# Performance work log

Hardware: AMD Instinct MI355X
Metric: run time of the kernel (lower is better)

Reference implementation:

```python
import jax, jax.numpy as jnp
import numpy as np

KH, KW = 3, 3
KK = KH * KW
PAD = 1
STRIDE = 1


def setup_inputs() -> dict:
    key = jax.random.key(0)
    k1, k2, k3 = jax.random.split(key, 3)
    x = jax.random.normal(k1, (4, 64, 224, 224), jnp.float32)
    weight = jax.random.normal(k2, (64, 64, KH, KW), jnp.float32) * 0.05
    bias = jax.random.normal(k3, (64,), jnp.float32)
    return {"x": x, "weight": weight, "bias": bias}


def reference(x, weight, bias):
    B, C, H, W = x.shape
    # --- conv output (the wrapper delegates this to the wrapped conv) ---
    y = jax.lax.conv_general_dilated(
        x, weight,
        window_strides=(STRIDE, STRIDE),
        padding=((PAD, PAD), (PAD, PAD)),
        dimension_numbers=("NCHW", "OIHW", "NCHW"),
    ) + bias[None, :, None, None]

    # --- zero-count histogram (groups=1; torch code's [:, :, :, 0, 0] indexing
    # selects group 0 / out-channel 0, so only weight[0] matters) ---
    # patches: (B, C*KK, Ho, Wo), channel-major ordering (channel, then kh, kw)
    patches = jax.lax.conv_general_dilated_patches(
        x, (KH, KW), (STRIDE, STRIDE), ((PAD, PAD), (PAD, PAD)))
    Ho, Wo = patches.shape[2], patches.shape[3]
    patches = patches.reshape(B, C, KK, Ho, Wo)
    prod = patches * weight[0].reshape(1, C, KK, 1, 1)  # patch * weight, oc=0
    # num_of_zeros = kk - count_nonzero over the kernel window
    zeros = KK - jnp.count_nonzero(prod, axis=2)  # (B, C, Ho, Wo), int
    # accumulate one_hot(zeros).sum over (batch, h, w) per input channel
    zf = zeros.transpose(1, 0, 2, 3).reshape(C, -1)  # (C, B*Ho*Wo)
    hist = jnp.zeros((C, KK + 1), jnp.float32).at[
        jnp.arange(C)[:, None], zf].add(1.0)
    return y, hist
```

## Files before the change

kernel.cpp:

```cpp
#include <hip/hip_runtime.h>

#define HW 224
#define HW2 50176
#define NCH 64
#define NPIX (4 * HW2)
#define CONV_OUT_ELEMS (4 * NCH * HW2)
#define ZCAP 8192

typedef short bf16x8 __attribute__((ext_vector_type(8)));
typedef float f32x4 __attribute__((ext_vector_type(4)));

__device__ __forceinline__ unsigned short f2bf(float f) {
    unsigned u = __float_as_uint(f);
    u += 0x7FFFu + ((u >> 16) & 1u);
    return (unsigned short)(u >> 16);
}


__global__ __launch_bounds__(256) void prep_weights_v2(
    const float* __restrict__ w, unsigned short* __restrict__ wbufA,
    int* __restrict__ zcnt) {
    const int o = blockIdx.x * 256 + threadIdx.x;
    if (o == 0) *zcnt = 0;
    if (o >= 18 * 2048) return;
    const int j    = o & 7;
    const int lane = (o >> 3) & 63;
    const int n    = lane & 15;
    const int q    = lane >> 4;
    const int mg   = (o >> 9) & 3;
    const int k    = o >> 11;
    const int tap  = k >> 1;
    const int half = k & 1;
    const int ci   = half * 32 + q * 8 + j;
    const int co   = mg * 16 + n;
    wbufA[o] = f2bf(w[(co * 64 + ci) * 9 + tap]);
}

__global__ __launch_bounds__(256, 3) void conv_fused(
    const float* __restrict__ xf,
    const unsigned short* __restrict__ wbufA,
    const float* __restrict__ bias, float* __restrict__ y,
    int* __restrict__ zcnt, unsigned int* __restrict__ zlist)
{
    __shared__ alignas(16) unsigned short xs[340 * 64];

    const int tid  = threadIdx.x;
    const int wv   = tid >> 6;
    const int lane = tid & 63;
    const int n    = lane & 15;
    const int q    = lane >> 4;
    const int c0   = blockIdx.x * 32;
    const int r0   = blockIdx.y * 8;
    const int b    = blockIdx.z;

    float fv[11][8];
#pragma unroll
    for (int it = 0; it < 11; ++it) {
        const int i   = tid + it * 256;
        const int ii  = i < 2720 ? i : 2719;
        const int oct = ii / 340;
        const int pos = ii - oct * 340;
        const int rr  = pos / 34;
        const int cc  = pos - rr * 34;
        const int gy  = r0 + rr - 1;
        const int gx  = c0 + cc - 1;
        const int cgy = min(max(gy, 0), HW - 1);
        const int cgx = min(max(gx, 0), HW - 1);
        const float* p =
            xf + ((size_t)(b * NCH + oct * 8) * HW + cgy) * HW + cgx;
#pragma unroll
        for (int j = 0; j < 8; ++j) fv[it][j] = p[(size_t)j * HW2];
    }
    __builtin_amdgcn_sched_barrier(0);

#pragma unroll
    for (int it = 0; it < 11; ++it) {
        const int i = tid + it * 256;
        if (i < 2720) {
            const int oct = i / 340;
            const int pos = i - oct * 340;
            const int rr  = pos / 34;
            const int cc  = pos - rr * 34;
            const int gy  = r0 + rr - 1;
            const int gx  = c0 + cc - 1;
            const bool inb =
                (unsigned)gy < (unsigned)HW && (unsigned)gx < (unsigned)HW;
            bf16x8 v;
            bool anyz = false;
#pragma unroll
            for (int j = 0; j < 8; ++j) {
                const float f = inb ? fv[it][j] : 0.0f;
                v[j] = (short)f2bf(f);
                anyz |= (f == 0.0f);
            }
            const int phys = pos * 8 + (oct ^ (pos & 7));
            *reinterpret_cast<bf16x8*>(xs + phys * 8) = v;
            if (__builtin_expect(
                    anyz && rr >= 1 && rr <= 8 && cc >= 1 && cc <= 32, 0)) {
#pragma unroll
                for (int j = 0; j < 8; ++j) {
                    if (fv[it][j] == 0.0f) {
                        const int idx = atomicAdd(zcnt, 1);
                        if (idx < ZCAP) {
                            const int ci = oct * 8 + j;
                            zlist[idx] = ((unsigned)b << 22)
                                       | ((unsigned)ci << 16)
                                       | ((unsigned)gy << 8) | (unsigned)gx;
                        }
                    }
                }
            }
        }
    }
    __syncthreads();

    f32x4 acc[4][4];
#pragma unroll
    for (int mg = 0; mg < 4; ++mg)
#pragma unroll
        for (int g = 0; g < 4; ++g) acc[mg][g] = (f32x4){0.f, 0.f, 0.f, 0.f};

#pragma unroll
    for (int tap = 0; tap < 9; ++tap) {
        const int dh = tap / 3, dw = tap % 3;
#pragma unroll
        for (int half = 0; half < 2; ++half) {
            const int k = tap * 2 + half;
            bf16x8 a[4];
#pragma unroll
            for (int mg = 0; mg < 4; ++mg)
                a[mg] = *reinterpret_cast<const bf16x8*>(
                    wbufA + (k * 4 + mg) * 512 + lane * 8);
#pragma unroll
            for (int g = 0; g < 4; ++g) {
                const int pos = (2 * wv + (g >> 1) + dh) * 34
                              + (g & 1) * 16 + dw + n;
                const int phys = pos * 8 + ((half * 4 + q) ^ (pos & 7));
                const bf16x8 bf =
                    *reinterpret_cast<const bf16x8*>(xs + phys * 8);
#pragma unroll
                for (int mg = 0; mg < 4; ++mg)
                    acc[mg][g] = __builtin_amdgcn_mfma_f32_16x16x32_bf16(
                        a[mg], bf, acc[mg][g], 0, 0, 0);
            }
        }
    }

#pragma unroll
    for (int g = 0; g < 4; ++g) {
        const int row = r0 + 2 * wv + (g >> 1);
        const int col = c0 + (g & 1) * 16 + n;
#pragma unroll
        for (int mg = 0; mg < 4; ++mg) {
#pragma unroll
            for (int rg = 0; rg < 4; ++rg) {
                const int co = mg * 16 + q * 4 + rg;
                y[((size_t)(b * NCH + co) * HW + row) * HW + col] =
                    acc[mg][g][rg] + bias[co];
            }
        }
    }
}

__global__ __launch_bounds__(256) void hist_final(
    const float* __restrict__ x, const float* __restrict__ w,
    const int* __restrict__ zcnt, const unsigned int* __restrict__ zlist,
    float* __restrict__ hist)
{
    __shared__ int lh[640];
    const int tid = threadIdx.x;
    for (int i = tid; i < 640; i += 256) lh[i] = 0;
    __syncthreads();

    if (tid < 64) {
        const int c = tid;
        float wk[9];
#pragma unroll
        for (int k = 0; k < 9; ++k) wk[k] = w[c * 9 + k];
        int bins[10];
#pragma unroll
        for (int k = 0; k < 10; ++k) bins[k] = 0;
#pragma unroll
        for (int rcat = 0; rcat < 3; ++rcat) {
#pragma unroll
            for (int scat = 0; scat < 3; ++scat) {
                int z = 0;
#pragma unroll
                for (int k = 0; k < 9; ++k) {
                    const int kh = k / 3, kw = k % 3;
                    const bool oob =
                        (rcat == 0 && kh == 0) || (rcat == 2 && kh == 2) ||
                        (scat == 0 && kw == 0) || (scat == 2 && kw == 2);
                    z += (oob || wk[k] == 0.0f) ? 1 : 0;
                }
                const int cnt =
                    4 * (rcat == 1 ? 222 : 1) * (scat == 1 ? 222 : 1);
                bins[z] += cnt;
            }
        }
#pragma unroll
        for (int k = 0; k < 10; ++k) lh[c * 10 + k] = bins[k];
    }
    __syncthreads();

    const int L = min(*zcnt, ZCAP);
    for (int p = tid; p < L * 9; p += 256) {
        const int e = p / 9, t = p - e * 9;
        const unsigned ent = zlist[e];
        const int b  = (int)(ent >> 22);
        const int c  = (int)(ent >> 16) & 63;
        const int zy = (int)(ent >> 8) & 255;
        const int zx = (int)ent & 255;
        const int kh = t / 3, kw = t % 3;
        const int r = zy - kh + 1, s = zx - kw + 1;
        if ((unsigned)r >= (unsigned)HW || (unsigned)s >= (unsigned)HW)
            continue;
        bool first = true;
        for (int e2 = 0; e2 < e && first; ++e2) {
            const unsigned ent2 = zlist[e2];
            if ((ent2 >> 16) == (ent >> 16)) {
                const int y2 = (int)(ent2 >> 8) & 255;
                const int x2 = (int)ent2 & 255;
                if ((unsigned)(y2 - r + 1) < 3u && (unsigned)(x2 - s + 1) < 3u)
                    first = false;
            }
        }
        if (!first) continue;

        const float* plane = x + (size_t)(b * NCH + c) * HW2;
        int zb = 0, zt = 0;
#pragma unroll
        for (int k = 0; k < 9; ++k) {
            const int kh2 = k / 3, kw2 = k % 3;
            const int yy = r + kh2 - 1, xx = s + kw2 - 1;
            const bool oob = (unsigned)yy >= (unsigned)HW ||
                             (unsigned)xx >= (unsigned)HW;
            const bool w0 = (w[c * 9 + k] == 0.0f);
            const bool x0 = !oob && (plane[yy * HW + xx] == 0.0f);
            zb += (oob || w0) ? 1 : 0;
            zt += (oob || w0 || x0) ? 1 : 0;
        }
        if (zb != zt) {
            atomicAdd(&lh[c * 10 + zb], -1);
            atomicAdd(&lh[c * 10 + zt], 1);
        }
    }
    __syncthreads();
    for (int i = tid; i < 640; i += 256) hist[i] = (float)lh[i];
}

__global__ void prep_weights_fb(const float* __restrict__ w,
                                unsigned short* __restrict__ wbuf) {
    const int o = blockIdx.x * 256 + threadIdx.x;
    if (o >= 2 * 9 * 4 * 16 * 32) return;
    const int ci = o & 31;
    const int t1 = o >> 5;
    const int co = t1 & 15;
    const int t2 = t1 >> 4;
    const int mg = t2 & 3;
    const int t3 = t2 >> 2;
    const int tap = t3 % 9;
    const int chunk = t3 / 9;
    wbuf[o] = f2bf(w[((mg * 16 + co) * 64 + (chunk * 32 + ci)) * 9 + tap]);
}

__global__ __launch_bounds__(256, 2) void conv_mfma_fb(
    const float* __restrict__ x, const unsigned short* __restrict__ wbuf,
    const float* __restrict__ bias, float* __restrict__ y)
{
    __shared__ alignas(16) unsigned short xs[340 * 32];
    const int tid  = threadIdx.x;
    const int wv   = tid >> 6;
    const int lane = tid & 63;
    const int n    = lane & 15;
    const int q    = lane >> 4;
    const int c0   = blockIdx.x * 32;
    const int r0   = blockIdx.y * 8;
    const int b    = blockIdx.z;

    f32x4 acc[4][4];
#pragma unroll
    for (int mg = 0; mg < 4; ++mg)
#pragma unroll
        for (int g = 0; g < 4; ++g) acc[mg][g] = (f32x4){0.f, 0.f, 0.f, 0.f};

    for (int chunk = 0; chunk < 2; ++chunk) {
        if (chunk) __syncthreads();
        const int ci0 = chunk * 32;
        for (int i = tid; i < 1360; i += 256) {
            const int ci8 = i / 340;
            const int pos = i - ci8 * 340;
            const int r   = pos / 34;
            const int c   = pos - r * 34;
            const int gy  = r0 + r - 1;
            const int gx  = c0 + c - 1;
            bf16x8 v;
            if ((unsigned)gy < (unsigned)HW && (unsigned)gx < (unsigned)HW) {
                const float* src =
                    x + ((size_t)(b * NCH + ci0 + ci8 * 8) * HW + gy) * HW + gx;
#pragma unroll
                for (int j = 0; j < 8; ++j) v[j] = (short)f2bf(src[(size_t)j * HW2]);
            } else {
#pragma unroll
                for (int j = 0; j < 8; ++j) v[j] = 0;
            }
            *reinterpret_cast<bf16x8*>(&xs[pos * 32 + ci8 * 8]) = v;
        }
        __syncthreads();

#pragma unroll
        for (int tap = 0; tap < 9; ++tap) {
            const int dh = tap / 3, dw = tap % 3;
            bf16x8 a[4];
#pragma unroll
            for (int mg = 0; mg < 4; ++mg) {
                const unsigned short* ap =
                    wbuf + ((chunk * 9 + tap) * 4 + mg) * 512 + n * 32 + q * 8;
                a[mg] = *reinterpret_cast<const bf16x8*>(ap);
            }
#pragma unroll
            for (int g = 0; g < 4; ++g) {
                const int rl = 2 * wv + (g >> 1) + dh;
                const int cl = (g & 1) * 16 + dw + n;
                const bf16x8 bf =
                    *reinterpret_cast<const bf16x8*>(&xs[(rl * 34 + cl) * 32 + q * 8]);
#pragma unroll
                for (int mg = 0; mg < 4; ++mg)
                    acc[mg][g] = __builtin_amdgcn_mfma_f32_16x16x32_bf16(
                        a[mg], bf, acc[mg][g], 0, 0, 0);
            }
        }
    }

#pragma unroll
    for (int g = 0; g < 4; ++g) {
        const int row = r0 + 2 * wv + (g >> 1);
        const int col = c0 + (g & 1) * 16 + n;
#pragma unroll
        for (int mg = 0; mg < 4; ++mg) {
#pragma unroll
            for (int rg = 0; rg < 4; ++rg) {
                const int co = mg * 16 + q * 4 + rg;
                y[((size_t)(b * NCH + co) * HW + row) * HW + col] =
                    acc[mg][g][rg] + bias[co];
            }
        }
    }
}

__global__ __launch_bounds__(256) void hist_v2(
    const float* __restrict__ x, const float* __restrict__ w,
    float* __restrict__ hist)
{
    __shared__ int lh[10];
    const int tid = threadIdx.x;
    const int col = tid;
    const int rg  = blockIdx.x;
    const int c   = blockIdx.y;
    const int b   = blockIdx.z;
    if (tid < 10) lh[tid] = 0;
    __syncthreads();

    int h[10];
#pragma unroll
    for (int k = 0; k < 10; ++k) h[k] = 0;

    if (col < HW) {
        const float* plane = x + (size_t)(b * NCH + c) * HW2;
        float wk[9];
#pragma unroll
        for (int k = 0; k < 9; ++k) wk[k] = w[c * 9 + k];

        const bool vl = col > 0, vr = col < HW - 1;
        const int r0 = rg * 28;
        float u0, u1, u2, m0, m1, m2;
        if (r0 > 0) {
            const float* p = plane + (size_t)(r0 - 1) * HW + col;
            u0 = vl ? p[-1] : 0.f; u1 = p[0]; u2 = vr ? p[1] : 0.f;
        } else { u0 = u1 = u2 = 0.f; }
        {
            const float* p = plane + (size_t)r0 * HW + col;
            m0 = vl ? p[-1] : 0.f; m1 = p[0]; m2 = vr ? p[1] : 0.f;
        }

        for (int r = r0; r < r0 + 28; ++r) {
            float d0, d1, d2;
            if (r + 1 < HW) {
                const float* p = plane + (size_t)(r + 1) * HW + col;
                d0 = vl ? p[-1] : 0.f; d1 = p[0]; d2 = vr ? p[1] : 0.f;
            } else { d0 = d1 = d2 = 0.f; }

            int cnt = 0;
            cnt += (u0 * wk[0] != 0.f); cnt += (u1 * wk[1] != 0.f); cnt += (u2 * wk[2] != 0.f);
            cnt += (m0 * wk[3] != 0.f); cnt += (m1 * wk[4] != 0.f); cnt += (m2 * wk[5] != 0.f);
            cnt += (d0 * wk[6] != 0.f); cnt += (d1 * wk[7] != 0.f); cnt += (d2 * wk[8] != 0.f);
            const int z = 9 - cnt;
#pragma unroll
            for (int k = 0; k < 10; ++k) h[k] += (z == k);
            u0 = m0; u1 = m1; u2 = m2; m0 = d0; m1 = d1; m2 = d2;
        }
    }

#pragma unroll
    for (int k = 0; k < 10; ++k) {
        int v = h[k];
        v += __shfl_xor(v, 32); v += __shfl_xor(v, 16); v += __shfl_xor(v, 8);
        v += __shfl_xor(v, 4);  v += __shfl_xor(v, 2);  v += __shfl_xor(v, 1);
        if ((tid & 63) == 0 && v != 0) atomicAdd(&lh[k], v);
    }
    __syncthreads();
    if (tid < 10 && lh[tid] > 0)
        atomicAdd(&hist[c * 10 + tid], (float)lh[tid]);
}

extern "C" void kernel_launch(void* const* d_in, const int* in_sizes, int n_in,
                              void* d_out, int out_size, void* d_ws, size_t ws_size,
                              hipStream_t stream) {
    const float* x    = (const float*)d_in[0];
    const float* w    = (const float*)d_in[1];
    const float* bias = (const float*)d_in[2];
    float* y    = (float*)d_out;
    float* hist = (float*)d_out + CONV_OUT_ELEMS;

    const size_t ZC_OFF = 73728;
    const size_t ZL_OFF = ZC_OFF + 64;
    const size_t NEED   = ZL_OFF + (size_t)ZCAP * 4;

    if (ws_size >= NEED) {
        unsigned short* wbufA = (unsigned short*)d_ws;
        int* zcnt             = (int*)((char*)d_ws + ZC_OFF);
        unsigned int* zlist   = (unsigned int*)((char*)d_ws + ZL_OFF);

        prep_weights_v2<<<144, 256, 0, stream>>>(w, wbufA, zcnt);
        conv_fused<<<dim3(7, 28, 4), 256, 0, stream>>>(
            x, wbufA, bias, y, zcnt, zlist);
        hist_final<<<1, 256, 0, stream>>>(x, w, zcnt, zlist, hist);
    } else {
        hipMemsetAsync(hist, 0, 64 * 10 * sizeof(float), stream);
        unsigned short* wbuf = (unsigned short*)d_ws;
        prep_weights_fb<<<144, 256, 0, stream>>>(w, wbuf);
        conv_mfma_fb<<<dim3(7, 28, 4), 256, 0, stream>>>(x, wbuf, bias, y);
        hist_v2<<<dim3(8, 64, 4), 256, 0, stream>>>(x, w, hist);
    }
}
```

Measured before the change: 131.8 us.

## Enlarge conv tile to 28x28 with 1024-thread blocks and 4x4 pixel MFMA units

Switches the fused conv from 8x32 output tiles per 256-thread block to 28x28 tiles per 1024-thread block, with each MFMA N-dimension covering a 4x4 pixel patch. The aim is to reduce halo overhead and redundant input loads per output. In exchange, LDS use rises to about 115KB per block, limiting residency to one block per CU. The work split across waves is uneven (49 units over 16 waves), and output stores become less contiguous.

```diff
diff --git a/kernel.cpp b/kernel.cpp
--- a/kernel.cpp
+++ b/kernel.cpp
@@ -6,6 +6,11 @@
 #define NPIX (4 * HW2)
 #define CONV_OUT_ELEMS (4 * NCH * HW2)
 #define ZCAP 8192
+
+#define TILE 28
+#define LW   30
+#define POS  (LW * LW)
+#define UNITS 49
 
 typedef short bf16x8 __attribute__((ext_vector_type(8)));
 typedef float f32x4 __attribute__((ext_vector_type(4)));
@@ -36,76 +41,81 @@
     wbufA[o] = f2bf(w[(co * 64 + ci) * 9 + tap]);
 }
 
-__global__ __launch_bounds__(256, 3) void conv_fused(
+__global__ __launch_bounds__(1024, 4) void conv_fused(
     const float* __restrict__ xf,
     const unsigned short* __restrict__ wbufA,
     const float* __restrict__ bias, float* __restrict__ y,
     int* __restrict__ zcnt, unsigned int* __restrict__ zlist)
 {
-    __shared__ alignas(16) unsigned short xs[340 * 64];
+    __shared__ alignas(16) unsigned short xs[POS * 64];
 
     const int tid  = threadIdx.x;
     const int wv   = tid >> 6;
     const int lane = tid & 63;
     const int n    = lane & 15;
     const int q    = lane >> 4;
-    const int c0   = blockIdx.x * 32;
-    const int r0   = blockIdx.y * 8;
+    const int rn   = n >> 2;
+    const int cn   = n & 3;
+    const int c0   = blockIdx.x * TILE;
+    const int r0   = blockIdx.y * TILE;
     const int b    = blockIdx.z;
 
-    float fv[11][8];
-#pragma unroll
-    for (int it = 0; it < 11; ++it) {
-        const int i   = tid + it * 256;
-        const int ii  = i < 2720 ? i : 2719;
-        const int oct = ii / 340;
-        const int pos = ii - oct * 340;
-        const int rr  = pos / 34;
-        const int cc  = pos - rr * 34;
-        const int gy  = r0 + rr - 1;
-        const int gx  = c0 + cc - 1;
-        const int cgy = min(max(gy, 0), HW - 1);
-        const int cgx = min(max(gx, 0), HW - 1);
-        const float* p =
-            xf + ((size_t)(b * NCH + oct * 8) * HW + cgy) * HW + cgx;
-#pragma unroll
-        for (int j = 0; j < 8; ++j) fv[it][j] = p[(size_t)j * HW2];
-    }
-    __builtin_amdgcn_sched_barrier(0);
-
-#pragma unroll
-    for (int it = 0; it < 11; ++it) {
-        const int i = tid + it * 256;
-        if (i < 2720) {
-            const int oct = i / 340;
-            const int pos = i - oct * 340;
-            const int rr  = pos / 34;
-            const int cc  = pos - rr * 34;
+#pragma unroll
+    for (int round = 0; round < 2; ++round) {
+        float fv[4][8];
+#pragma unroll
+        for (int it = 0; it < 4; ++it) {
+            const int i   = tid + (round * 4 + it) * 1024;
+            const int ii  = i < 7200 ? i : 7199;
+            const int oct = ii / POS;
+            const int pos = ii - oct * POS;
+            const int rr  = pos / LW;
+            const int cc  = pos - rr * LW;
             const int gy  = r0 + rr - 1;
             const int gx  = c0 + cc - 1;
-            const bool inb =
-                (unsigned)gy < (unsigned)HW && (unsigned)gx < (unsigned)HW;
-            bf16x8 v;
-            bool anyz = false;
-#pragma unroll
-            for (int j = 0; j < 8; ++j) {
-                const float f = inb ? fv[it][j] : 0.0f;
-                v[j] = (short)f2bf(f);
-                anyz |= (f == 0.0f);
-            }
-            const int phys = pos * 8 + (oct ^ (pos & 7));
-            *reinterpret_cast<bf16x8*>(xs + phys * 8) = v;
-            if (__builtin_expect(
-                    anyz && rr >= 1 && rr <= 8 && cc >= 1 && cc <= 32, 0)) {
+            const int cgy = min(max(gy, 0), HW - 1);
+            const int cgx = min(max(gx, 0), HW - 1);
+            const float* p =
+                xf + ((size_t)(b * NCH + oct * 8) * HW + cgy) * HW + cgx;
+#pragma unroll
+            for (int j = 0; j < 8; ++j) fv[it][j] = p[(size_t)j * HW2];
+        }
+        __builtin_amdgcn_sched_barrier(0);
+#pragma unroll
+        for (int it = 0; it < 4; ++it) {
+            const int i = tid + (round * 4 + it) * 1024;
+            if (i < 7200) {
+                const int oct = i / POS;
+                const int pos = i - oct * POS;
+                const int rr  = pos / LW;
+                const int cc  = pos - rr * LW;
+                const int gy  = r0 + rr - 1;
+                const int gx  = c0 + cc - 1;
+                const bool inb = (unsigned)gy < (unsigned)HW &&
+                                 (unsigned)gx < (unsigned)HW;
+                bf16x8 v;
+                bool anyz = false;
 #pragma unroll
                 for (int j = 0; j < 8; ++j) {
-                    if (fv[it][j] == 0.0f) {
-                        const int idx = atomicAdd(zcnt, 1);
-                        if (idx < ZCAP) {
-                            const int ci = oct * 8 + j;
-                            zlist[idx] = ((unsigned)b << 22)
-                                       | ((unsigned)ci << 16)
-                                       | ((unsigned)gy << 8) | (unsigned)gx;
+                    const float f = inb ? fv[it][j] : 0.0f;
+                    v[j] = (short)f2bf(f);
+                    anyz |= (f == 0.0f);
+                }
+                const int phys = pos * 8 + (oct ^ (pos & 7));
+                *reinterpret_cast<bf16x8*>(xs + phys * 8) = v;
+                if (__builtin_expect(anyz && rr >= 1 && rr <= TILE &&
+                                     cc >= 1 && cc <= TILE, 0)) {
+#pragma unroll
+                    for (int j = 0; j < 8; ++j) {
+                        if (fv[it][j] == 0.0f) {
+                            const int idx = atomicAdd(zcnt, 1);
+                            if (idx < ZCAP) {
+                                const int ci = oct * 8 + j;
+                                zlist[idx] = ((unsigned)b << 22)
+                                           | ((unsigned)ci << 16)
+                                           | ((unsigned)gy << 8)
+                                           | (unsigned)gx;
+                            }
                         }
                     }
                 }
@@ -116,9 +126,9 @@
 
     f32x4 acc[4][4];
 #pragma unroll
-    for (int mg = 0; mg < 4; ++mg)
-#pragma unroll
-        for (int g = 0; g < 4; ++g) acc[mg][g] = (f32x4){0.f, 0.f, 0.f, 0.f};
+    for (int t = 0; t < 4; ++t)
+#pragma unroll
+        for (int mg = 0; mg < 4; ++mg) acc[t][mg] = (f32x4){0.f, 0.f, 0.f, 0.f};
 
 #pragma unroll
     for (int tap = 0; tap < 9; ++tap) {
@@ -132,31 +142,39 @@
                 a[mg] = *reinterpret_cast<const bf16x8*>(
                     wbufA + (k * 4 + mg) * 512 + lane * 8);
 #pragma unroll
-            for (int g = 0; g < 4; ++g) {
-                const int pos = (2 * wv + (g >> 1) + dh) * 34
-                              + (g & 1) * 16 + dw + n;
-                const int phys = pos * 8 + ((half * 4 + q) ^ (pos & 7));
-                const bf16x8 bf =
-                    *reinterpret_cast<const bf16x8*>(xs + phys * 8);
-#pragma unroll
-                for (int mg = 0; mg < 4; ++mg)
-                    acc[mg][g] = __builtin_amdgcn_mfma_f32_16x16x32_bf16(
-                        a[mg], bf, acc[mg][g], 0, 0, 0);
-            }
-        }
-    }
-
-#pragma unroll
-    for (int g = 0; g < 4; ++g) {
-        const int row = r0 + 2 * wv + (g >> 1);
-        const int col = c0 + (g & 1) * 16 + n;
-#pragma unroll
-        for (int mg = 0; mg < 4; ++mg) {
-#pragma unroll
-            for (int rg = 0; rg < 4; ++rg) {
-                const int co = mg * 16 + q * 4 + rg;
-                y[((size_t)(b * NCH + co) * HW + row) * HW + col] =
-                    acc[mg][g][rg] + bias[co];
+            for (int t = 0; t < 4; ++t) {
+                const int u = wv + 16 * t;
+                if (u < UNITS) {
+                    const int ur = u / 7, uc = u - ur * 7;
+                    const int pos = (ur * 4 + rn + dh) * LW
+                                  + uc * 4 + cn + dw;
+                    const int phys = pos * 8 + ((half * 4 + q) ^ (pos & 7));
+                    const bf16x8 bf =
+                        *reinterpret_cast<const bf16x8*>(xs + phys * 8);
+#pragma unroll
+                    for (int mg = 0; mg < 4; ++mg)
+                        acc[t][mg] = __builtin_amdgcn_mfma_f32_16x16x32_bf16(
+                            a[mg], bf, acc[t][mg], 0, 0, 0);
+                }
+            }
+        }
+    }
+
+#pragma unroll
+    for (int t = 0; t < 4; ++t) {
+        const int u = wv + 16 * t;
+        if (u < UNITS) {
+            const int ur = u / 7, uc = u - ur * 7;
+            const int row = r0 + ur * 4 + rn;
+            const int col = c0 + uc * 4 + cn;
+#pragma unroll
+            for (int mg = 0; mg < 4; ++mg) {
+#pragma unroll
+                for (int rg = 0; rg < 4; ++rg) {
+                    const int co = mg * 16 + q * 4 + rg;
+                    y[((size_t)(b * NCH + co) * HW + row) * HW + col] =
+                        acc[t][mg][rg] + bias[co];
+                }
             }
         }
     }
@@ -432,7 +450,7 @@
         unsigned int* zlist   = (unsigned int*)((char*)d_ws + ZL_OFF);
 
         prep_weights_v2<<<144, 256, 0, stream>>>(w, wbufA, zcnt);
-        conv_fused<<<dim3(7, 28, 4), 256, 0, stream>>>(
+        conv_fused<<<dim3(8, 8, 4), 1024, 0, stream>>>(
             x, wbufA, bias, y, zcnt, zlist);
         hist_final<<<1, 256, 0, stream>>>(x, w, zcnt, zlist, hist);
     } else {
```

Result: slower. 138.0 us (+4.7%).

## Shrink conv tile width to 28 and stage loads in two rounds for occupancy

Applied to the files above, without the earlier changes.

The conv tile narrows from 32 to 28 columns, so the LDS buffer shrinks (304 positions instead of 340). The staging loads are split into two rounds of five instead of one batch of eleven, which cuts register pressure. Together these let launch bounds rise to 4 blocks per CU, and the grid goes to 8x28x4. The cost is that the second 16-column MFMA group computes 4 wasted columns, and halo loads are a larger share of each tile.

```diff
diff --git a/kernel.cpp b/kernel.cpp
--- a/kernel.cpp
+++ b/kernel.cpp
@@ -6,6 +6,13 @@
 #define NPIX (4 * HW2)
 #define CONV_OUT_ELEMS (4 * NCH * HW2)
 #define ZCAP 8192
+
+#define TH 8
+#define TW 28
+#define LH 10
+#define LWW 30
+#define NPOS 300
+#define XSPOS 304
 
 typedef short bf16x8 __attribute__((ext_vector_type(8)));
 typedef float f32x4 __attribute__((ext_vector_type(4)));
@@ -36,76 +43,79 @@
     wbufA[o] = f2bf(w[(co * 64 + ci) * 9 + tap]);
 }
 
-__global__ __launch_bounds__(256, 3) void conv_fused(
+__global__ __launch_bounds__(256, 4) void conv_fused(
     const float* __restrict__ xf,
     const unsigned short* __restrict__ wbufA,
     const float* __restrict__ bias, float* __restrict__ y,
     int* __restrict__ zcnt, unsigned int* __restrict__ zlist)
 {
-    __shared__ alignas(16) unsigned short xs[340 * 64];
+    __shared__ alignas(16) unsigned short xs[XSPOS * 64];
 
     const int tid  = threadIdx.x;
     const int wv   = tid >> 6;
     const int lane = tid & 63;
     const int n    = lane & 15;
     const int q    = lane >> 4;
-    const int c0   = blockIdx.x * 32;
-    const int r0   = blockIdx.y * 8;
+    const int c0   = blockIdx.x * TW;
+    const int r0   = blockIdx.y * TH;
     const int b    = blockIdx.z;
 
-    float fv[11][8];
-#pragma unroll
-    for (int it = 0; it < 11; ++it) {
-        const int i   = tid + it * 256;
-        const int ii  = i < 2720 ? i : 2719;
-        const int oct = ii / 340;
-        const int pos = ii - oct * 340;
-        const int rr  = pos / 34;
-        const int cc  = pos - rr * 34;
-        const int gy  = r0 + rr - 1;
-        const int gx  = c0 + cc - 1;
-        const int cgy = min(max(gy, 0), HW - 1);
-        const int cgx = min(max(gx, 0), HW - 1);
-        const float* p =
-            xf + ((size_t)(b * NCH + oct * 8) * HW + cgy) * HW + cgx;
-#pragma unroll
-        for (int j = 0; j < 8; ++j) fv[it][j] = p[(size_t)j * HW2];
-    }
-    __builtin_amdgcn_sched_barrier(0);
-
-#pragma unroll
-    for (int it = 0; it < 11; ++it) {
-        const int i = tid + it * 256;
-        if (i < 2720) {
-            const int oct = i / 340;
-            const int pos = i - oct * 340;
-            const int rr  = pos / 34;
-            const int cc  = pos - rr * 34;
+#pragma unroll
+    for (int round = 0; round < 2; ++round) {
+        float fv[5][8];
+#pragma unroll
+        for (int it = 0; it < 5; ++it) {
+            const int i   = tid + (round * 5 + it) * 256;
+            const int ii  = i < 2400 ? i : 2399;
+            const int oct = ii / NPOS;
+            const int pos = ii - oct * NPOS;
+            const int rr  = pos / LWW;
+            const int cc  = pos - rr * LWW;
             const int gy  = r0 + rr - 1;
             const int gx  = c0 + cc - 1;
-            const bool inb =
-                (unsigned)gy < (unsigned)HW && (unsigned)gx < (unsigned)HW;
-            bf16x8 v;
-            bool anyz = false;
-#pragma unroll
-            for (int j = 0; j < 8; ++j) {
-                const float f = inb ? fv[it][j] : 0.0f;
-                v[j] = (short)f2bf(f);
-                anyz |= (f == 0.0f);
-            }
-            const int phys = pos * 8 + (oct ^ (pos & 7));
-            *reinterpret_cast<bf16x8*>(xs + phys * 8) = v;
-            if (__builtin_expect(
-                    anyz && rr >= 1 && rr <= 8 && cc >= 1 && cc <= 32, 0)) {
+            const int cgy = min(max(gy, 0), HW - 1);
+            const int cgx = min(max(gx, 0), HW - 1);
+            const float* p =
+                xf + ((size_t)(b * NCH + oct * 8) * HW + cgy) * HW + cgx;
+#pragma unroll
+            for (int j = 0; j < 8; ++j) fv[it][j] = p[(size_t)j * HW2];
+        }
+        __builtin_amdgcn_sched_barrier(0);
+#pragma unroll
+        for (int it = 0; it < 5; ++it) {
+            const int i = tid + (round * 5 + it) * 256;
+            if (i < 2400) {
+                const int oct = i / NPOS;
+                const int pos = i - oct * NPOS;
+                const int rr  = pos / LWW;
+                const int cc  = pos - rr * LWW;
+                const int gy  = r0 + rr - 1;
+                const int gx  = c0 + cc - 1;
+                const bool inb = (unsigned)gy < (unsigned)HW &&
+                                 (unsigned)gx < (unsigned)HW;
+                bf16x8 v;
+                bool anyz = false;
 #pragma unroll
                 for (int j = 0; j < 8; ++j) {
-                    if (fv[it][j] == 0.0f) {
-                        const int idx = atomicAdd(zcnt, 1);
-                        if (idx < ZCAP) {
-                            const int ci = oct * 8 + j;
-                            zlist[idx] = ((unsigned)b << 22)
-                                       | ((unsigned)ci << 16)
-                                       | ((unsigned)gy << 8) | (unsigned)gx;
+                    const float f = inb ? fv[it][j] : 0.0f;
+                    v[j] = (short)f2bf(f);
+                    anyz |= (f == 0.0f);
+                }
+                const int phys = pos * 8 + (oct ^ (pos & 7));
+                *reinterpret_cast<bf16x8*>(xs + phys * 8) = v;
+                if (__builtin_expect(anyz && rr >= 1 && rr <= TH &&
+                                     cc >= 1 && cc <= TW, 0)) {
+#pragma unroll
+                    for (int j = 0; j < 8; ++j) {
+                        if (fv[it][j] == 0.0f) {
+                            const int idx = atomicAdd(zcnt, 1);
+                            if (idx < ZCAP) {
+                                const int ci = oct * 8 + j;
+                                zlist[idx] = ((unsigned)b << 22)
+                                           | ((unsigned)ci << 16)
+                                           | ((unsigned)gy << 8)
+                                           | (unsigned)gx;
+                            }
                         }
                     }
                 }
@@ -133,7 +143,7 @@
                     wbufA + (k * 4 + mg) * 512 + lane * 8);
 #pragma unroll
             for (int g = 0; g < 4; ++g) {
-                const int pos = (2 * wv + (g >> 1) + dh) * 34
+                const int pos = (2 * wv + (g >> 1) + dh) * LWW
                               + (g & 1) * 16 + dw + n;
                 const int phys = pos * 8 + ((half * 4 + q) ^ (pos & 7));
                 const bf16x8 bf =
@@ -150,13 +160,15 @@
     for (int g = 0; g < 4; ++g) {
         const int row = r0 + 2 * wv + (g >> 1);
         const int col = c0 + (g & 1) * 16 + n;
-#pragma unroll
-        for (int mg = 0; mg < 4; ++mg) {
-#pragma unroll
-            for (int rg = 0; rg < 4; ++rg) {
-                const int co = mg * 16 + q * 4 + rg;
-                y[((size_t)(b * NCH + co) * HW + row) * HW + col] =
-                    acc[mg][g][rg] + bias[co];
+        if ((g & 1) == 0 || n < TW - 16) {
+#pragma unroll
+            for (int mg = 0; mg < 4; ++mg) {
+#pragma unroll
+                for (int rg = 0; rg < 4; ++rg) {
+                    const int co = mg * 16 + q * 4 + rg;
+                    y[((size_t)(b * NCH + co) * HW + row) * HW + col] =
+                        acc[mg][g][rg] + bias[co];
+                }
             }
         }
     }
@@ -432,7 +444,7 @@
         unsigned int* zlist   = (unsigned int*)((char*)d_ws + ZL_OFF);
 
         prep_weights_v2<<<144, 256, 0, stream>>>(w, wbufA, zcnt);
-        conv_fused<<<dim3(7, 28, 4), 256, 0, stream>>>(
+        conv_fused<<<dim3(8, 28, 4), 256, 0, stream>>>(
             x, wbufA, bias, y, zcnt, zlist);
         hist_final<<<1, 256, 0, stream>>>(x, w, zcnt, zlist, hist);
     } else {
```

After: 184.8 us. 1.4x slower.
